# Optimization experiments

Hardware: AMD Instinct MI355X
Metric: run time of the kernel (lower is better)

Reference implementation:

```python
import jax, jax.numpy as jnp
import numpy as np

HEADS = 8
EPS = 1e-5


def setup_inputs() -> dict:
    key = jax.random.key(0)
    ks = jax.random.split(key, 8)
    B, S, D = 4, 2048, 512
    inputs = jax.random.normal(ks[0], (B, S, D), dtype=jnp.float32)
    mask = jnp.ones((B, S), dtype=jnp.int32)
    sc = 1.0 / np.sqrt(D)
    # torch Linear weights stored transposed as [in, out] for x @ W
    W_qkv = jax.random.uniform(ks[1], (D, 3 * D), jnp.float32, -sc, sc)
    b_qkv = jax.random.uniform(ks[2], (3 * D,), jnp.float32, -sc, sc)
    W_o = jax.random.uniform(ks[3], (D, D), jnp.float32, -sc, sc)
    b_o = jax.random.uniform(ks[4], (D,), jnp.float32, -sc, sc)
    gamma = jnp.ones((D,), jnp.float32)
    beta = jnp.zeros((D,), jnp.float32)
    return {"inputs": inputs, "mask": mask, "W_qkv": W_qkv, "b_qkv": b_qkv,
            "W_o": W_o, "b_o": b_o, "gamma": gamma, "beta": beta}


def reference(inputs, mask, W_qkv, b_qkv, W_o, b_o, gamma, beta):
    B, S, D = inputs.shape
    H = HEADS
    dh = D // H
    t = inputs @ W_qkv + b_qkv                      # [B,S,3D]
    q, k, v = jnp.split(t, 3, axis=-1)
    # [B,S,D] -> [B,H,S,dh]
    q = q.reshape(B, S, H, dh).transpose(0, 2, 1, 3)
    k = k.reshape(B, S, H, dh).transpose(0, 2, 1, 3)
    v = v.reshape(B, S, H, dh).transpose(0, 2, 1, 3)
    # unscaled dot-product attention (is_scaled=False in the source)
    scores = jnp.einsum('bhqd,bhkd->bhqk', q, k)    # [B,H,S,S]
    key_mask = (mask > 0)[:, None, None, :]         # broadcast over heads & query rows
    scores = jnp.where(key_mask, scores, -jnp.inf)
    attn = jax.nn.softmax(scores, axis=-1)
    att = jnp.einsum('bhqk,bhkd->bhqd', attn, v)    # [B,H,S,dh]
    att = att.transpose(0, 2, 1, 3).reshape(B, S, D)
    out = att @ W_o + b_o
    x = out + att                                    # residual
    mu = jnp.mean(x, axis=-1, keepdims=True)
    var = jnp.mean(jnp.square(x - mu), axis=-1, keepdims=True)
    return (x - mu) / jnp.sqrt(var + EPS) * gamma + beta
```

## Files before the change

### kernel.cpp

```cpp
#include <hip/hip_runtime.h>
#include <cstdint>

#define S_LEN 2048
#define D_MODEL 512
#define H_NUM 8
#define DH 64
#define LOG2E 1.4426950408889634f

typedef __attribute__((ext_vector_type(8))) short bf16x8;
typedef __attribute__((ext_vector_type(8))) unsigned short u16x8;
typedef __attribute__((ext_vector_type(4))) float f32x4;

__device__ inline unsigned short f2bf(float x) {
    unsigned int u = __builtin_bit_cast(unsigned int, x);
    u += 0x7fffu + ((u >> 16) & 1u);
    return (unsigned short)(u >> 16);
}
__device__ inline float bf2f(unsigned short u) {
    return __builtin_bit_cast(float, (unsigned int)u << 16);
}

__device__ inline void async_ld16(const unsigned short* g, unsigned short* l) {
    __builtin_amdgcn_global_load_lds(
        (const __attribute__((address_space(1))) unsigned int*)(const unsigned int*)g,
        (__attribute__((address_space(3))) unsigned int*)(unsigned int*)l,
        16, 0, 0);
}

__global__ __launch_bounds__(256) void prep(
    const float* __restrict__ X, const float* __restrict__ Wqkv,
    const float* __restrict__ Wo,
    unsigned short* __restrict__ Xb, unsigned short* __restrict__ WqkvT,
    unsigned short* __restrict__ WoT)
{
    __shared__ float tile[32][36];
    const int blk = blockIdx.x;
    const int tid = threadIdx.x;
    if (blk < 1024) {
        const int base = blk * 4096 + tid * 16;
        #pragma unroll
        for (int i = 0; i < 4; ++i) {
            float4 v = *(const float4*)(X + base + i * 4);
            ushort4 o;
            o.x = f2bf(v.x); o.y = f2bf(v.y); o.z = f2bf(v.z); o.w = f2bf(v.w);
            *(ushort4*)(Xb + base + i * 4) = o;
        }
        return;
    }
    const float* src; unsigned short* dst; int N, t;
    if (blk < 1792) { src = Wqkv; dst = WqkvT; N = 1536; t = blk - 1024; }
    else            { src = Wo;   dst = WoT;   N = 512;  t = blk - 1792; }
    const int tnx = N / 32;
    const int bx = t % tnx;
    const int by = t / tnx;
    const int row = tid >> 3;
    const int c4  = (tid & 7) * 4;
    *(float4*)&tile[row][c4] = *(const float4*)(src + (size_t)(by * 32 + row) * N + bx * 32 + c4);
    __syncthreads();
    ushort4 o;
    o.x = f2bf(tile[c4 + 0][row]);
    o.y = f2bf(tile[c4 + 1][row]);
    o.z = f2bf(tile[c4 + 2][row]);
    o.w = f2bf(tile[c4 + 3][row]);
    *(ushort4*)(dst + (size_t)(bx * 32 + row) * 512 + by * 32 + c4) = o;
}

__global__ __launch_bounds__(256) void qkv_mfma(
    const unsigned short* __restrict__ Xb, const unsigned short* __restrict__ WT,
    const float* __restrict__ bias,
    unsigned short* __restrict__ Q, unsigned short* __restrict__ K,
    unsigned short* __restrict__ Vt)
{
    __shared__ unsigned short sA[128 * 64];
    __shared__ unsigned short sB[128 * 64];
    const int tid  = threadIdx.x;
    const int w    = tid >> 6;
    const int lane = tid & 63;
    const int l16  = lane & 15;
    const int quad = lane >> 4;
    const int wm = w >> 1, wn = w & 1;
    const int n0 = blockIdx.x * 128;
    const int m0 = blockIdx.y * 128;

    const unsigned short* gA[4]; const unsigned short* gB[4];
    unsigned short *lA[4], *lB[4];
    #pragma unroll
    for (int j = 0; j < 4; ++j) {
        const int ci = tid + j * 256;
        const int row = ci >> 3;
        const int col = ((ci & 7) ^ (row & 7)) * 8;
        gA[j] = Xb + (size_t)(m0 + row) * 512 + col;
        gB[j] = WT + (size_t)(n0 + row) * 512 + col;
        lA[j] = sA + ci * 8 - lane * 8;
        lB[j] = sB + ci * 8 - lane * 8;
    }

    f32x4 acc[4][4] = {};
    for (int k0 = 0; k0 < 512; k0 += 64) {
        __syncthreads();
        #pragma unroll
        for (int j = 0; j < 4; ++j) {
            async_ld16(gA[j] + k0, lA[j]);
            async_ld16(gB[j] + k0, lB[j]);
        }
        __syncthreads();
        bf16x8 a[4][2], bfr[4][2];
        #pragma unroll
        for (int mi = 0; mi < 4; ++mi) {
            const int row = wm * 64 + mi * 16 + l16;
            a[mi][0] = *(const bf16x8*)&sA[row * 64 + ((quad       ^ (row & 7)) * 8)];
            a[mi][1] = *(const bf16x8*)&sA[row * 64 + (((4 + quad) ^ (row & 7)) * 8)];
        }
        #pragma unroll
        for (int ni = 0; ni < 4; ++ni) {
            const int row = wn * 64 + ni * 16 + l16;
            bfr[ni][0] = *(const bf16x8*)&sB[row * 64 + ((quad       ^ (row & 7)) * 8)];
            bfr[ni][1] = *(const bf16x8*)&sB[row * 64 + (((4 + quad) ^ (row & 7)) * 8)];
        }
        #pragma unroll
        for (int mi = 0; mi < 4; ++mi)
            #pragma unroll
            for (int ni = 0; ni < 4; ++ni) {
                acc[mi][ni] = __builtin_amdgcn_mfma_f32_16x16x32_bf16(a[mi][0], bfr[ni][0], acc[mi][ni], 0, 0, 0);
                acc[mi][ni] = __builtin_amdgcn_mfma_f32_16x16x32_bf16(a[mi][1], bfr[ni][1], acc[mi][ni], 0, 0, 0);
            }
    }

    const int which = n0 >> 9;
    const int h = ((n0 & 511) >> 6) + wn;
    const int b = m0 >> 11;
    const int sbase = (m0 & 2047) + wm * 64;
    float bv[4];
    #pragma unroll
    for (int ni = 0; ni < 4; ++ni) bv[ni] = bias[n0 + wn * 64 + ni * 16 + l16];
    if (which == 2) {
        #pragma unroll
        for (int ni = 0; ni < 4; ++ni) {
            const int dh = ni * 16 + l16;
            unsigned short* vp = Vt + ((size_t)(b * H_NUM + h) * DH + dh) * S_LEN;
            #pragma unroll
            for (int mi = 0; mi < 4; ++mi) {
                const int s0 = sbase + mi * 16 + quad * 4;
                ushort4 o;
                o.x = f2bf(acc[mi][ni][0] + bv[ni]);
                o.y = f2bf(acc[mi][ni][1] + bv[ni]);
                o.z = f2bf(acc[mi][ni][2] + bv[ni]);
                o.w = f2bf(acc[mi][ni][3] + bv[ni]);
                *(ushort4*)(vp + s0) = o;
            }
        }
    } else {
        const float qs = (which == 0) ? LOG2E : 1.0f;
        unsigned short* dst = (which == 0) ? Q : K;
        dst += (size_t)(b * H_NUM + h) * S_LEN * DH;
        #pragma unroll
        for (int mi = 0; mi < 4; ++mi)
            #pragma unroll
            for (int r = 0; r < 4; ++r) {
                const int s = sbase + mi * 16 + quad * 4 + r;
                #pragma unroll
                for (int ni = 0; ni < 4; ++ni)
                    dst[(size_t)s * DH + ni * 16 + l16] = f2bf((acc[mi][ni][r] + bv[ni]) * qs);
            }
    }
}

__global__ __launch_bounds__(256) void attn_mfma(
    const unsigned short* __restrict__ Q, const unsigned short* __restrict__ K,
    const unsigned short* __restrict__ Vt, const int* __restrict__ mask,
    unsigned short* __restrict__ att)
{
    __shared__ unsigned short sK[64 * 64];
    __shared__ unsigned short sVt[64 * 64];
    __shared__ unsigned short sP[4][32][72];
    __shared__ float smbt[64];

    const int tid  = threadIdx.x;
    const int w    = tid >> 6;
    const int lane = tid & 63;
    const int l16  = lane & 15;
    const int quad = lane >> 4;
    const int qt = blockIdx.x;
    const int bh = blockIdx.y;
    const int b  = bh >> 3;
    const int h  = bh & 7;
    const size_t kbase = (size_t)bh * S_LEN * DH;
    const size_t vbase = (size_t)bh * DH * S_LEN;

    bf16x8 qf[2][2];
    {
        const unsigned short* qp = Q + kbase + (size_t)(qt * 128 + w * 16 + l16) * DH + quad * 8;
        qf[0][0] = *(const bf16x8*)qp;
        qf[0][1] = *(const bf16x8*)(qp + 32);
        qf[1][0] = *(const bf16x8*)(qp + 64 * DH);
        qf[1][1] = *(const bf16x8*)(qp + 64 * DH + 32);
    }

    const int ci0 = w * 128 + lane;
    const int ci1 = ci0 + 64;
    const int r0_ = ci0 >> 3, c0_ = ((ci0 & 7) ^ (r0_ & 7)) * 8;
    const int r1_ = ci1 >> 3, c1_ = ((ci1 & 7) ^ (r1_ & 7)) * 8;
    const int kOff0 = r0_ * 64 + c0_;
    const int kOff1 = r1_ * 64 + c1_;
    const int vOff0 = r0_ * S_LEN + c0_;
    const int vOff1 = r1_ * S_LEN + c1_;
    const int lds0 = ci0 * 8 - lane * 8;
    const int lds1 = ci1 * 8 - lane * 8;

    f32x4 O[2][4] = {};
    float lacc[2] = {0.f, 0.f};

    for (int kt = 0; kt < 32; ++kt) {
        __syncthreads();
        {
            const unsigned short* gK = K  + kbase + (size_t)kt * 64 * DH;
            const unsigned short* gV = Vt + vbase + kt * 64;
            async_ld16(gK + kOff0, sK + lds0);
            async_ld16(gK + kOff1, sK + lds1);
            async_ld16(gV + vOff0, sVt + lds0);
            async_ld16(gV + vOff1, sVt + lds1);
            if (tid < 64) smbt[tid] = mask[b * S_LEN + kt * 64 + tid] ? 0.f : -1e30f;
        }
        __syncthreads();

        bf16x8 kb[4][2];
        #pragma unroll
        for (int nb = 0; nb < 4; ++nb) {
            const int row = nb * 16 + l16;
            const int x = row & 7;
            kb[nb][0] = *(const bf16x8*)&sK[row * 64 + ((quad       ^ x) * 8)];
            kb[nb][1] = *(const bf16x8*)&sK[row * 64 + (((4 + quad) ^ x) * 8)];
        }
        float4 mb[4];
        #pragma unroll
        for (int nb = 0; nb < 4; ++nb)
            mb[nb] = *(const float4*)&smbt[nb * 16 + quad * 4];

        #pragma unroll
        for (int t = 0; t < 2; ++t) {
            f32x4 c[4] = {{0,0,0,0},{0,0,0,0},{0,0,0,0},{0,0,0,0}};
            #pragma unroll
            for (int nb = 0; nb < 4; ++nb) {
                c[nb] = __builtin_amdgcn_mfma_f32_16x16x32_bf16(kb[nb][0], qf[t][0], c[nb], 0, 0, 0);
                c[nb] = __builtin_amdgcn_mfma_f32_16x16x32_bf16(kb[nb][1], qf[t][1], c[nb], 0, 0, 0);
            }
            float ls = 0.f;
            #pragma unroll
            for (int nb = 0; nb < 4; ++nb) {
                const float p0 = __builtin_amdgcn_exp2f(c[nb][0] + mb[nb].x);
                const float p1 = __builtin_amdgcn_exp2f(c[nb][1] + mb[nb].y);
                const float p2 = __builtin_amdgcn_exp2f(c[nb][2] + mb[nb].z);
                const float p3 = __builtin_amdgcn_exp2f(c[nb][3] + mb[nb].w);
                ls += (p0 + p1) + (p2 + p3);
                ushort4 pk;
                pk.x = f2bf(p0); pk.y = f2bf(p1); pk.z = f2bf(p2); pk.w = f2bf(p3);
                *(ushort4*)&sP[w][t * 16 + l16][nb * 16 + quad * 4] = pk;
            }
            lacc[t] += ls;
        }

        bf16x8 vb[4][2];
        #pragma unroll
        for (int db = 0; db < 4; ++db) {
            const int row = db * 16 + l16;
            const int x = row & 7;
            vb[db][0] = *(const bf16x8*)&sVt[row * 64 + ((quad       ^ x) * 8)];
            vb[db][1] = *(const bf16x8*)&sVt[row * 64 + (((4 + quad) ^ x) * 8)];
        }
        #pragma unroll
        for (int t = 0; t < 2; ++t) {
            const bf16x8 pa0 = *(const bf16x8*)&sP[w][t * 16 + l16][quad * 8];
            const bf16x8 pa1 = *(const bf16x8*)&sP[w][t * 16 + l16][quad * 8 + 32];
            #pragma unroll
            for (int db = 0; db < 4; ++db) {
                O[t][db] = __builtin_amdgcn_mfma_f32_16x16x32_bf16(pa0, vb[db][0], O[t][db], 0, 0, 0);
                O[t][db] = __builtin_amdgcn_mfma_f32_16x16x32_bf16(pa1, vb[db][1], O[t][db], 0, 0, 0);
            }
        }
    }

    #pragma unroll
    for (int t = 0; t < 2; ++t) {
        float l = lacc[t];
        l += __shfl_xor(l, 16, 64);
        l += __shfl_xor(l, 32, 64);
        #pragma unroll
        for (int r = 0; r < 4; ++r) {
            const float invr = 1.0f / __shfl(l, quad * 4 + r, 16);
            const size_t grow = (size_t)b * S_LEN + qt * 128 + t * 64 + w * 16 + quad * 4 + r;
            unsigned short* op = att + grow * D_MODEL + h * DH + l16;
            op[0]  = f2bf(O[t][0][r] * invr);
            op[16] = f2bf(O[t][1][r] * invr);
            op[32] = f2bf(O[t][2][r] * invr);
            op[48] = f2bf(O[t][3][r] * invr);
        }
    }
}

__global__ __launch_bounds__(256) void proj_mfma(
    const unsigned short* __restrict__ attb, const unsigned short* __restrict__ WoT,
    const float* __restrict__ bo, float* __restrict__ xbuf)
{
    __shared__ unsigned short sA[128 * 64];
    __shared__ unsigned short sB[64 * 64];
    const int tid  = threadIdx.x;
    const int w    = tid >> 6;
    const int lane = tid & 63;
    const int l16  = lane & 15;
    const int quad = lane >> 4;
    const int wm = w >> 1, wn = w & 1;
    const int n0 = blockIdx.x * 64;
    const int m0 = blockIdx.y * 128;

    const unsigned short* gA[4]; unsigned short* lA[4];
    const unsigned short* gB[2]; unsigned short* lB[2];
    #pragma unroll
    for (int j = 0; j < 4; ++j) {
        const int ci = tid + j * 256;
        const int row = ci >> 3;
        const int col = ((ci & 7) ^ (row & 7)) * 8;
        gA[j] = attb + (size_t)(m0 + row) * 512 + col;
        lA[j] = sA + ci * 8 - lane * 8;
    }
    #pragma unroll
    for (int j = 0; j < 2; ++j) {
        const int ci = tid + j * 256;
        const int row = ci >> 3;
        const int col = ((ci & 7) ^ (row & 7)) * 8;
        gB[j] = WoT + (size_t)(n0 + row) * 512 + col;
        lB[j] = sB + ci * 8 - lane * 8;
    }

    f32x4 acc[4][2] = {};
    for (int k0 = 0; k0 < 512; k0 += 64) {
        __syncthreads();
        #pragma unroll
        for (int j = 0; j < 4; ++j) async_ld16(gA[j] + k0, lA[j]);
        #pragma unroll
        for (int j = 0; j < 2; ++j) async_ld16(gB[j] + k0, lB[j]);
        __syncthreads();
        bf16x8 a[4][2], bfr[2][2];
        #pragma unroll
        for (int mi = 0; mi < 4; ++mi) {
            const int row = wm * 64 + mi * 16 + l16;
            a[mi][0] = *(const bf16x8*)&sA[row * 64 + ((quad       ^ (row & 7)) * 8)];
            a[mi][1] = *(const bf16x8*)&sA[row * 64 + (((4 + quad) ^ (row & 7)) * 8)];
        }
        #pragma unroll
        for (int ni = 0; ni < 2; ++ni) {
            const int row = wn * 32 + ni * 16 + l16;
            bfr[ni][0] = *(const bf16x8*)&sB[row * 64 + ((quad       ^ (row & 7)) * 8)];
            bfr[ni][1] = *(const bf16x8*)&sB[row * 64 + (((4 + quad) ^ (row & 7)) * 8)];
        }
        #pragma unroll
        for (int mi = 0; mi < 4; ++mi)
            #pragma unroll
            for (int ni = 0; ni < 2; ++ni) {
                acc[mi][ni] = __builtin_amdgcn_mfma_f32_16x16x32_bf16(a[mi][0], bfr[ni][0], acc[mi][ni], 0, 0, 0);
                acc[mi][ni] = __builtin_amdgcn_mfma_f32_16x16x32_bf16(a[mi][1], bfr[ni][1], acc[mi][ni], 0, 0, 0);
            }
    }

    #pragma unroll
    for (int ni = 0; ni < 2; ++ni) {
        const int n = n0 + wn * 32 + ni * 16 + l16;
        const float bv = bo[n];
        #pragma unroll
        for (int mi = 0; mi < 4; ++mi) {
            #pragma unroll
            for (int r = 0; r < 4; ++r) {
                const int m = m0 + wm * 64 + mi * 16 + quad * 4 + r;
                const float resid = bf2f(attb[(size_t)m * 512 + n]);
                xbuf[(size_t)m * 512 + n] = acc[mi][ni][r] + bv + resid;
            }
        }
    }
}

__global__ __launch_bounds__(256) void ln_kernel(
    const float* __restrict__ xbuf, const float* __restrict__ gamma,
    const float* __restrict__ beta, float* __restrict__ out)
{
    const int tid = threadIdx.x;
    const int w = tid >> 6, lane = tid & 63;
    const size_t row = (size_t)blockIdx.x * 4 + w;
    const float* xp = xbuf + row * 512 + lane * 8;
    float4 v0 = *(const float4*)xp;
    float4 v1 = *(const float4*)(xp + 4);
    float s  = v0.x + v0.y + v0.z + v0.w + v1.x + v1.y + v1.z + v1.w;
    float sq = v0.x*v0.x + v0.y*v0.y + v0.z*v0.z + v0.w*v0.w
             + v1.x*v1.x + v1.y*v1.y + v1.z*v1.z + v1.w*v1.w;
    #pragma unroll
    for (int off = 1; off < 64; off <<= 1) {
        s  += __shfl_xor(s, off, 64);
        sq += __shfl_xor(sq, off, 64);
    }
    const float mu = s * (1.0f / 512.0f);
    const float var = sq * (1.0f / 512.0f) - mu * mu;
    const float rs = rsqrtf(var + 1e-5f);
    float4 g0 = *(const float4*)(gamma + lane * 8);
    float4 g1 = *(const float4*)(gamma + lane * 8 + 4);
    float4 b0 = *(const float4*)(beta + lane * 8);
    float4 b1 = *(const float4*)(beta + lane * 8 + 4);
    float4 o0, o1;
    o0.x = (v0.x - mu) * rs * g0.x + b0.x;
    o0.y = (v0.y - mu) * rs * g0.y + b0.y;
    o0.z = (v0.z - mu) * rs * g0.z + b0.z;
    o0.w = (v0.w - mu) * rs * g0.w + b0.w;
    o1.x = (v1.x - mu) * rs * g1.x + b1.x;
    o1.y = (v1.y - mu) * rs * g1.y + b1.y;
    o1.z = (v1.z - mu) * rs * g1.z + b1.z;
    o1.w = (v1.w - mu) * rs * g1.w + b1.w;
    float* op = out + row * 512 + lane * 8;
    *(float4*)op = o0;
    *(float4*)(op + 4) = o1;
}

extern "C" void kernel_launch(void* const* d_in, const int* in_sizes, int n_in,
                              void* d_out, int out_size, void* d_ws, size_t ws_size,
                              hipStream_t stream)
{
    (void)in_sizes; (void)n_in; (void)out_size; (void)ws_size;
    const float* X    = (const float*)d_in[0];
    const int*   mask = (const int*)d_in[1];
    const float* Wqkv = (const float*)d_in[2];
    const float* bqkv = (const float*)d_in[3];
    const float* Wo   = (const float*)d_in[4];
    const float* bo   = (const float*)d_in[5];
    const float* gamma= (const float*)d_in[6];
    const float* beta = (const float*)d_in[7];
    float* out = (float*)d_out;

    const size_t NE = (size_t)4 * S_LEN * D_MODEL;
    unsigned short* ws16 = (unsigned short*)d_ws;
    unsigned short* Xb     = ws16;
    unsigned short* WqkvT  = Xb + NE;
    unsigned short* WoT    = WqkvT + 786432;
    unsigned short* Q      = WoT + 262144;
    unsigned short* K      = Q + NE;
    unsigned short* Vt     = K + NE;
    unsigned short* attb   = Vt + NE;
    float* xbuf = (float*)(attb + NE);

    prep<<<dim3(2048), 256, 0, stream>>>(X, Wqkv, Wo, Xb, WqkvT, WoT);
    qkv_mfma<<<dim3(12, 64), 256, 0, stream>>>(Xb, WqkvT, bqkv, Q, K, Vt);
    attn_mfma<<<dim3(16, 32), 256, 0, stream>>>(Q, K, Vt, mask, attb);
    proj_mfma<<<dim3(8, 64), 256, 0, stream>>>(attb, WoT, bo, xbuf);
    ln_kernel<<<dim3(2048), 256, 0, stream>>>(xbuf, gamma, beta, out);
}
```

Measured before the change: 185.5 us.

## Double-buffer K/V tiles in attention and compute row sums via MFMA

The attention kernel now double-buffers the K, V^T and mask tiles in LDS, issuing the async loads for the next key tile before computing on the current one and dropping one barrier per iteration. This is meant to hide global-load latency. The softmax row sum moves from scalar adds plus shuffles to extra MFMAs against a ones vector, and the bf16 packing uses a cheaper round-half-up with a perm instruction. The row sum is now taken over the bf16-rounded probabilities and LDS use grows. With only one barrier per iteration, a tile may be overwritten while still being read, and the loads are not explicitly waited on.

New measurement: 181.9 us. About the same (-1.9%).

```diff
diff --git a/kernel.cpp b/kernel.cpp
--- a/kernel.cpp
+++ b/kernel.cpp
@@ -18,6 +18,11 @@
 }
 __device__ inline float bf2f(unsigned short u) {
     return __builtin_bit_cast(float, (unsigned int)u << 16);
+}
+__device__ inline unsigned pack_bf2(float a, float b) {
+    unsigned ua = __builtin_bit_cast(unsigned, a) + 0x8000u;
+    unsigned ub = __builtin_bit_cast(unsigned, b) + 0x8000u;
+    return __builtin_amdgcn_perm(ub, ua, 0x07060302);
 }
 
 __device__ inline void async_ld16(const unsigned short* g, unsigned short* l) {
@@ -170,10 +175,10 @@
     const unsigned short* __restrict__ Vt, const int* __restrict__ mask,
     unsigned short* __restrict__ att)
 {
-    __shared__ unsigned short sK[64 * 64];
-    __shared__ unsigned short sVt[64 * 64];
+    __shared__ unsigned short sK[2][64 * 64];
+    __shared__ unsigned short sVt[2][64 * 64];
     __shared__ unsigned short sP[4][32][72];
-    __shared__ float smbt[64];
+    __shared__ float smbt[2][64];
 
     const int tid  = threadIdx.x;
     const int w    = tid >> 6;
@@ -207,34 +212,50 @@
     const int lds0 = ci0 * 8 - lane * 8;
     const int lds1 = ci1 * 8 - lane * 8;
 
+    bf16x8 vones;
+    #pragma unroll
+    for (int j = 0; j < 8; ++j) vones[j] = (short)0x3F80;
+
     f32x4 O[2][4] = {};
-    float lacc[2] = {0.f, 0.f};
+    f32x4 Ol[2] = {};
+
+    {
+        const unsigned short* gK = K  + kbase;
+        const unsigned short* gV = Vt + vbase;
+        async_ld16(gK + kOff0, sK[0] + lds0);
+        async_ld16(gK + kOff1, sK[0] + lds1);
+        async_ld16(gV + vOff0, sVt[0] + lds0);
+        async_ld16(gV + vOff1, sVt[0] + lds1);
+        if (tid < 64) smbt[0][tid] = mask[b * S_LEN + tid] ? 0.f : -1e30f;
+    }
 
     for (int kt = 0; kt < 32; ++kt) {
+        const int cur = kt & 1, nxt = cur ^ 1;
         __syncthreads();
-        {
-            const unsigned short* gK = K  + kbase + (size_t)kt * 64 * DH;
-            const unsigned short* gV = Vt + vbase + kt * 64;
-            async_ld16(gK + kOff0, sK + lds0);
-            async_ld16(gK + kOff1, sK + lds1);
-            async_ld16(gV + vOff0, sVt + lds0);
-            async_ld16(gV + vOff1, sVt + lds1);
-            if (tid < 64) smbt[tid] = mask[b * S_LEN + kt * 64 + tid] ? 0.f : -1e30f;
-        }
-        __syncthreads();
+        if (kt + 1 < 32) {
+            const unsigned short* gK = K  + kbase + (size_t)(kt + 1) * 64 * DH;
+            const unsigned short* gV = Vt + vbase + (kt + 1) * 64;
+            async_ld16(gK + kOff0, sK[nxt] + lds0);
+            async_ld16(gK + kOff1, sK[nxt] + lds1);
+            async_ld16(gV + vOff0, sVt[nxt] + lds0);
+            async_ld16(gV + vOff1, sVt[nxt] + lds1);
+            if (tid < 64) smbt[nxt][tid] = mask[b * S_LEN + (kt + 1) * 64 + tid] ? 0.f : -1e30f;
+        }
+        const unsigned short* sKc  = sK[cur];
+        const unsigned short* sVtc = sVt[cur];
 
         bf16x8 kb[4][2];
         #pragma unroll
         for (int nb = 0; nb < 4; ++nb) {
             const int row = nb * 16 + l16;
             const int x = row & 7;
-            kb[nb][0] = *(const bf16x8*)&sK[row * 64 + ((quad       ^ x) * 8)];
-            kb[nb][1] = *(const bf16x8*)&sK[row * 64 + (((4 + quad) ^ x) * 8)];
+            kb[nb][0] = *(const bf16x8*)&sKc[row * 64 + ((quad       ^ x) * 8)];
+            kb[nb][1] = *(const bf16x8*)&sKc[row * 64 + (((4 + quad) ^ x) * 8)];
         }
         float4 mb[4];
         #pragma unroll
         for (int nb = 0; nb < 4; ++nb)
-            mb[nb] = *(const float4*)&smbt[nb * 16 + quad * 4];
+            mb[nb] = *(const float4*)&smbt[cur][nb * 16 + quad * 4];
 
         #pragma unroll
         for (int t = 0; t < 2; ++t) {
@@ -244,19 +265,17 @@
                 c[nb] = __builtin_amdgcn_mfma_f32_16x16x32_bf16(kb[nb][0], qf[t][0], c[nb], 0, 0, 0);
                 c[nb] = __builtin_amdgcn_mfma_f32_16x16x32_bf16(kb[nb][1], qf[t][1], c[nb], 0, 0, 0);
             }
-            float ls = 0.f;
             #pragma unroll
             for (int nb = 0; nb < 4; ++nb) {
                 const float p0 = __builtin_amdgcn_exp2f(c[nb][0] + mb[nb].x);
                 const float p1 = __builtin_amdgcn_exp2f(c[nb][1] + mb[nb].y);
                 const float p2 = __builtin_amdgcn_exp2f(c[nb][2] + mb[nb].z);
                 const float p3 = __builtin_amdgcn_exp2f(c[nb][3] + mb[nb].w);
-                ls += (p0 + p1) + (p2 + p3);
-                ushort4 pk;
-                pk.x = f2bf(p0); pk.y = f2bf(p1); pk.z = f2bf(p2); pk.w = f2bf(p3);
-                *(ushort4*)&sP[w][t * 16 + l16][nb * 16 + quad * 4] = pk;
-            }
-            lacc[t] += ls;
+                uint2 pk;
+                pk.x = pack_bf2(p0, p1);
+                pk.y = pack_bf2(p2, p3);
+                *(uint2*)&sP[w][t * 16 + l16][nb * 16 + quad * 4] = pk;
+            }
         }
 
         bf16x8 vb[4][2];
@@ -264,8 +283,8 @@
         for (int db = 0; db < 4; ++db) {
             const int row = db * 16 + l16;
             const int x = row & 7;
-            vb[db][0] = *(const bf16x8*)&sVt[row * 64 + ((quad       ^ x) * 8)];
-            vb[db][1] = *(const bf16x8*)&sVt[row * 64 + (((4 + quad) ^ x) * 8)];
+            vb[db][0] = *(const bf16x8*)&sVtc[row * 64 + ((quad       ^ x) * 8)];
+            vb[db][1] = *(const bf16x8*)&sVtc[row * 64 + (((4 + quad) ^ x) * 8)];
         }
         #pragma unroll
         for (int t = 0; t < 2; ++t) {
@@ -276,17 +295,16 @@
                 O[t][db] = __builtin_amdgcn_mfma_f32_16x16x32_bf16(pa0, vb[db][0], O[t][db], 0, 0, 0);
                 O[t][db] = __builtin_amdgcn_mfma_f32_16x16x32_bf16(pa1, vb[db][1], O[t][db], 0, 0, 0);
             }
+            Ol[t] = __builtin_amdgcn_mfma_f32_16x16x32_bf16(pa0, vones, Ol[t], 0, 0, 0);
+            Ol[t] = __builtin_amdgcn_mfma_f32_16x16x32_bf16(pa1, vones, Ol[t], 0, 0, 0);
         }
     }
 
     #pragma unroll
     for (int t = 0; t < 2; ++t) {
-        float l = lacc[t];
-        l += __shfl_xor(l, 16, 64);
-        l += __shfl_xor(l, 32, 64);
         #pragma unroll
         for (int r = 0; r < 4; ++r) {
-            const float invr = 1.0f / __shfl(l, quad * 4 + r, 16);
+            const float invr = 1.0f / Ol[t][r];
             const size_t grow = (size_t)b * S_LEN + qt * 128 + t * 64 + w * 16 + quad * 4 + r;
             unsigned short* op = att + grow * D_MODEL + h * DH + l16;
             op[0]  = f2bf(O[t][0][r] * invr);
```
